# Performance work log

Hardware: AMD Instinct MI355X
Metric: run time of the kernel (lower is better)

Reference implementation:

```python
import jax, jax.numpy as jnp
import numpy as np
import math

NUM_HEADS = 16
HIDDEN = 1024
MLP = 4096
SEQ = 2048
HEAD_DIM = HIDDEN // NUM_HEADS  # 64
EPS = 1e-5


def setup_inputs() -> dict:
    key = jax.random.key(0)
    ks = jax.random.split(key, 16)
    s = 0.02
    inp = {
        "x": jax.random.normal(ks[0], (SEQ, HIDDEN), jnp.float32),
        "rope_cos": jnp.cos(jnp.arange(SEQ, dtype=jnp.float32)[:, None] * (1.0 / (10000.0 ** (jnp.arange(HEAD_DIM // 2, dtype=jnp.float32) * 2 / HEAD_DIM)))[None, :]),
        "rope_sin": jnp.sin(jnp.arange(SEQ, dtype=jnp.float32)[:, None] * (1.0 / (10000.0 ** (jnp.arange(HEAD_DIM // 2, dtype=jnp.float32) * 2 / HEAD_DIM)))[None, :]),
        "norm0_w": jnp.ones((HIDDEN,), jnp.float32),
        "norm0_b": jnp.zeros((HIDDEN,), jnp.float32),
        "norm1_w": jnp.ones((HIDDEN,), jnp.float32),
        "norm1_b": jnp.zeros((HIDDEN,), jnp.float32),
        "wqkv_w": jax.random.normal(ks[1], (3 * HIDDEN, HIDDEN), jnp.float32) * s,
        "wqkv_b": jnp.zeros((3 * HIDDEN,), jnp.float32),
        "wo_w": jax.random.normal(ks[2], (HIDDEN, HIDDEN), jnp.float32) * s,
        "wo_b": jnp.zeros((HIDDEN,), jnp.float32),
        "up_w": jax.random.normal(ks[3], (MLP, HIDDEN), jnp.float32) * s,
        "up_b": jnp.zeros((MLP,), jnp.float32),
        "down_w": jax.random.normal(ks[4], (HIDDEN, MLP), jnp.float32) * s,
        "down_b": jnp.zeros((HIDDEN,), jnp.float32),
        # 4 packed sequences of length 512 each
        "input_row_offsets": jnp.array([0, 512, 1024, 1536, 2048], jnp.int32),
    }
    return inp


def _layernorm(x, w, b):
    m = jnp.mean(x, axis=-1, keepdims=True)
    v = jnp.mean((x - m) ** 2, axis=-1, keepdims=True)
    return (x - m) * jax.lax.rsqrt(v + EPS) * w + b


def _rope(t, cos, sin):
    # t: [S, nh, hd]; cos/sin: [S, hd/2] -> complex rotation of adjacent pairs
    S, nh, hd = t.shape
    t2 = t.reshape(S, nh, hd // 2, 2)
    re, im = t2[..., 0], t2[..., 1]
    c = cos[:, None, :]
    s = sin[:, None, :]
    out = jnp.stack([re * c - im * s, re * s + im * c], axis=-1)
    return out.reshape(S, nh, hd)


def _block(x, rope_cos, rope_sin, norm0_w, norm0_b, wqkv_w, wqkv_b, wo_w, wo_b,
           up_w, up_b, down_w, down_b, norm1_w, norm1_b, input_row_offsets):
    S, H = x.shape
    nh, hd = NUM_HEADS, HEAD_DIM
    h = _layernorm(x, norm0_w, norm0_b)
    qkv = (h @ wqkv_w.T + wqkv_b).reshape(S, 3, nh, hd)
    q, k, v = qkv[:, 0], qkv[:, 1], qkv[:, 2]
    q = _rope(q, rope_cos, rope_sin)
    k = _rope(k, rope_cos, rope_sin)
    # block-diagonal bool mask added as 0/1 float (matches torch `attn_weight += bool_mask`)
    seg = jnp.searchsorted(input_row_offsets, jnp.arange(S), side="right") - 1
    mask = (seg[:, None] == seg[None, :]).astype(jnp.float32)  # [S, S]
    scores = jnp.einsum("shd,thd->hst", q, k) / math.sqrt(hd) + mask[None]
    attn = jax.nn.softmax(scores.astype(jnp.float32), axis=-1).astype(q.dtype)
    out = jnp.einsum("hst,thd->shd", attn, v).reshape(S, H)
    x = x + (out @ wo_w.T + wo_b)
    h = _layernorm(x, norm1_w, norm1_b)
    h = jax.nn.gelu(h @ up_w.T + up_b, approximate=True)
    return x + (h @ down_w.T + down_b)


def reference(x, rope_cos, rope_sin, norm0_w, norm0_b, norm1_w, norm1_b,
              wqkv_w, wqkv_b, wo_w, wo_b, up_w, up_b, down_w, down_b,
              input_row_offsets):
    return _block(x, rope_cos, rope_sin, norm0_w, norm0_b, wqkv_w, wqkv_b,
                  wo_w, wo_b, up_w, up_b, down_w, down_b, norm1_w, norm1_b,
                  input_row_offsets)
```

## Files before the change

kernel.cpp:

```cpp
#include <hip/hip_runtime.h>
#include <hip/hip_bf16.h>
#include <math.h>

#define SEQ 2048
#define HID 1024
#define NH 16
#define HD 64

using f32x4  = __attribute__((ext_vector_type(4))) float;
using bf16x8 = __attribute__((ext_vector_type(8))) short;

union U8 { unsigned int u[4]; bf16x8 v; short s[8]; };

__device__ __forceinline__ short f2bf(float f) {
  unsigned int x = __float_as_uint(f);
  unsigned int r = (x + 0x7fffu + ((x >> 16) & 1u)) >> 16;
  return (short)(r & 0xffffu);
}

__device__ __forceinline__ unsigned int pkbf(float a, float b) {
  return ((unsigned int)(unsigned short)f2bf(a)) |
         (((unsigned int)(unsigned short)f2bf(b)) << 16);
}

__device__ __forceinline__ float bf2f_lo(unsigned int u) {
  return __uint_as_float((u & 0xffffu) << 16);
}
__device__ __forceinline__ float bf2f_hi(unsigned int u) {
  return __uint_as_float(u & 0xffff0000u);
}

__device__ __forceinline__ float fast_exp2(float x) {
#if __has_builtin(__builtin_amdgcn_exp2f)
  return __builtin_amdgcn_exp2f(x);
#else
  return exp2f(x);
#endif
}

__device__ __forceinline__ float fast_rcp(float x) {
#if __has_builtin(__builtin_amdgcn_rcpf)
  return __builtin_amdgcn_rcpf(x);
#else
  return 1.0f / x;
#endif
}

__device__ __forceinline__ void async_cp16(const void* g, void* l) {
  __builtin_amdgcn_global_load_lds(
      (__attribute__((address_space(1))) void*)(g),
      (__attribute__((address_space(3))) void*)(l), 16, 0, 0);
}

__global__ void cvt_all_kernel(const float* __restrict__ a, const float* __restrict__ b,
                               const float* __restrict__ c, const float* __restrict__ d,
                               short* __restrict__ oa, short* __restrict__ ob,
                               short* __restrict__ oc, short* __restrict__ od) {
  int i = blockIdx.x * blockDim.x + threadIdx.x;
  const float* src; short* dst; int off;
  if (i < 786432)        { src = a; dst = oa; off = i; }
  else if (i < 1048576)  { src = b; dst = ob; off = i - 786432; }
  else if (i < 2097152)  { src = c; dst = oc; off = i - 1048576; }
  else                   { src = d; dst = od; off = i - 2097152; }
  float4 v = ((const float4*)src)[off];
  short4 o;
  o.x = f2bf(v.x); o.y = f2bf(v.y); o.z = f2bf(v.z); o.w = f2bf(v.w);
  ((short4*)dst)[off] = o;
}

__global__ __launch_bounds__(256) void ln_kernel(const float* __restrict__ x,
    const float* __restrict__ w, const float* __restrict__ b, short* __restrict__ out) {
  int row = blockIdx.x;
  int tid = threadIdx.x;
  float4 v = ((const float4*)(x + (size_t)row * HID))[tid];
  float s  = v.x + v.y + v.z + v.w;
  float s2 = v.x*v.x + v.y*v.y + v.z*v.z + v.w*v.w;
#pragma unroll
  for (int o = 32; o >= 1; o >>= 1) {
    s  += __shfl_xor(s,  o);
    s2 += __shfl_xor(s2, o);
  }
  __shared__ float red[8];
  int wv = tid >> 6;
  if ((tid & 63) == 0) { red[wv] = s; red[4 + wv] = s2; }
  __syncthreads();
  float ts  = red[0] + red[1] + red[2] + red[3];
  float ts2 = red[4] + red[5] + red[6] + red[7];
  float mean = ts * (1.0f / HID);
  float var  = ts2 * (1.0f / HID) - mean * mean;
  float rs = rsqrtf(var + 1e-5f);
  float4 wv4 = ((const float4*)w)[tid];
  float4 bv4 = ((const float4*)b)[tid];
  short4 o;
  o.x = f2bf((v.x - mean) * rs * wv4.x + bv4.x);
  o.y = f2bf((v.y - mean) * rs * wv4.y + bv4.y);
  o.z = f2bf((v.z - mean) * rs * wv4.z + bv4.z);
  o.w = f2bf((v.w - mean) * rs * wv4.w + bv4.w);
  ((short4*)(out + (size_t)row * HID))[tid] = o;
}

__global__ void rope_qk_kernel(const short* __restrict__ qkvb,
    const float* __restrict__ cosb, const float* __restrict__ sinb,
    short* __restrict__ Qh, short* __restrict__ Kh) {
  int tid = blockIdx.x * blockDim.x + threadIdx.x;
  int s   = tid >> 10;
  int r   = tid & 1023;
  int j   = r >> 9;
  int rem = r & 511;
  int h   = rem >> 5;
  int i   = rem & 31;
  int d   = i * 2;
  unsigned int u = *(const unsigned int*)(qkvb + (size_t)s * 3072 + j * 1024 + h * 64 + d);
  float a = bf2f_lo(u), b = bf2f_hi(u);
  float c  = cosb[s * 32 + i];
  float sn = sinb[s * 32 + i];
  float scale = (j == 0) ? 0.18033688011112043f : 1.0f;
  unsigned int o = pkbf(scale * (a * c - b * sn), scale * (a * sn + b * c));
  short* dst = (j == 0 ? Qh : Kh) + ((size_t)h * SEQ + s) * HD + d;
  *(unsigned int*)dst = o;
}

__global__ __launch_bounds__(256) void vtrans_kernel(const short* __restrict__ qkvb,
                                                     short* __restrict__ Vt) {
  __shared__ short tile[64 * 72];
  int s0   = blockIdx.x * 64;
  int head = blockIdx.y;
  int tid  = threadIdx.x;
#pragma unroll
  for (int p = 0; p < 2; p++) {
    int seg = p * 256 + tid;
    int row = seg >> 3;
    int c8  = seg & 7;
    bf16x8 v = *(const bf16x8*)(qkvb + (size_t)(s0 + row) * 3072 + 2048 + head * 64 + c8 * 8);
    *(bf16x8*)(tile + row * 72 + c8 * 8) = v;
  }
  __syncthreads();
#pragma unroll
  for (int p = 0; p < 2; p++) {
    int seg = p * 256 + tid;
    int d   = seg >> 3;
    int sc  = seg & 7;
    U8 o;
#pragma unroll
    for (int j = 0; j < 8; j++) o.s[j] = tile[(sc * 8 + j) * 72 + d];
    *(bf16x8*)(Vt + ((size_t)head * HD + d) * SEQ + s0 + sc * 8) = o.v;
  }
}

template <int EPI>
__global__ __launch_bounds__(256) void gemm_bt_kernel(
    const short* __restrict__ A, const short* __restrict__ B,
    const float* __restrict__ bias, const float* __restrict__ resid,
    void* __restrict__ outp, int M, int N, int Klen, int Kstride) {
  __shared__ __attribute__((aligned(16))) short Alds[128 * 32];
  __shared__ __attribute__((aligned(16))) short Blds[128 * 32];
  int tid = threadIdx.x;
  int w    = tid >> 6;
  int lane = tid & 63;
  int lcol  = lane & 15;
  int lhalf = lane >> 4;
  int m0 = blockIdx.y * 128;
  int n0 = blockIdx.x * 128;
  int z  = blockIdx.z;
  int wm = (w & 1) * 64;
  int wn = (w >> 1) * 64;

  const short* apt[2];
  const short* bpt[2];
#pragma unroll
  for (int p = 0; p < 2; p++) {
    int seg = p * 256 + tid;
    int row = seg >> 2;
    int c   = (seg & 3) ^ ((row >> 1) & 3);
    apt[p] = A + (size_t)z * Klen + (size_t)(m0 + row) * Kstride + c * 8;
    bpt[p] = B + (size_t)z * Klen + (size_t)(n0 + row) * Kstride + c * 8;
  }
  int sw = (lhalf ^ ((lcol >> 1) & 3)) * 8;

  f32x4 acc[4][4];
#pragma unroll
  for (int i = 0; i < 4; i++)
#pragma unroll
    for (int j = 0; j < 4; j++) acc[i][j] = (f32x4){0.f, 0.f, 0.f, 0.f};

  for (int k0 = 0; k0 < Klen; k0 += 32) {
#pragma unroll
    for (int p = 0; p < 2; p++) {
      async_cp16(apt[p], Alds + p * 2048 + w * 512);  apt[p] += 32;
      async_cp16(bpt[p], Blds + p * 2048 + w * 512);  bpt[p] += 32;
    }
    __syncthreads();
    bf16x8 af[4], bfr[4];
#pragma unroll
    for (int i = 0; i < 4; i++)
      af[i] = *(const bf16x8*)(Alds + (wm + i * 16 + lcol) * 32 + sw);
#pragma unroll
    for (int j = 0; j < 4; j++)
      bfr[j] = *(const bf16x8*)(Blds + (wn + j * 16 + lcol) * 32 + sw);
#pragma unroll
    for (int i = 0; i < 4; i++)
#pragma unroll
      for (int j = 0; j < 4; j++)
        acc[i][j] = __builtin_amdgcn_mfma_f32_16x16x32_bf16(af[i], bfr[j], acc[i][j], 0, 0, 0);
    __syncthreads();
  }

  float* outf = (float*)outp + (EPI == 4 ? (size_t)z * M * N : 0);
#pragma unroll
  for (int i = 0; i < 4; i++) {
#pragma unroll
    for (int j = 0; j < 4; j++) {
#pragma unroll
      for (int r = 0; r < 4; r++) {
        int row = m0 + wm + i * 16 + lhalf * 4 + r;
        int col = n0 + wn + j * 16 + lcol;
        float v = acc[i][j][r];
        if (EPI != 4) v += bias[col];
        if (EPI == 2) {
          float t = v * (1.5957691216057308f + 0.07135481283942279f * v * v);
          float e = fast_exp2(t * -1.4426950408889634f);
          v = v * fast_rcp(1.0f + e);
          ((short*)outp)[(size_t)row * N + col] = f2bf(v);
        } else if (EPI == 3) {
          ((short*)outp)[(size_t)row * N + col] = f2bf(v);
        } else {
          outf[(size_t)row * N + col] = v;
        }
      }
    }
  }
}

__global__ __launch_bounds__(256) void attn_kernel(
    const short* __restrict__ Qh, const short* __restrict__ Kh,
    const short* __restrict__ Vt, const int* __restrict__ offs,
    float* __restrict__ Opart, float* __restrict__ Lpart) {
  __shared__ __attribute__((aligned(16))) short Klds[64 * 64];
  __shared__ __attribute__((aligned(16))) short Vlds[64 * 64];
  __shared__ __attribute__((aligned(16))) unsigned int Plds[4][16 * 34];
  int head = blockIdx.y;
  int q0   = blockIdx.x * 64;
  int z    = blockIdx.z;
  int tid  = threadIdx.x;
  int w    = tid >> 6;
  int lane = tid & 63;
  int lcol = lane & 15;
  int h    = lane >> 4;
  int o1 = offs[1], o2 = offs[2], o3 = offs[3];

  int qrow = q0 + w * 16 + lcol;
  const short* qb = Qh + ((size_t)head * SEQ + qrow) * HD;
  bf16x8 qf0 = *(const bf16x8*)(qb + h * 8);
  bf16x8 qf1 = *(const bf16x8*)(qb + 32 + h * 8);
  int sq = (qrow >= o1) + (qrow >= o2) + (qrow >= o3);
  U8 qe;
  qe.u[0] = 0; qe.u[1] = 0; qe.u[2] = 0; qe.u[3] = 0;
  if (h == 0) qe.s[sq] = (short)0x3FB9;
  bf16x8 qf2 = qe.v;

  bf16x8 ones;
#pragma unroll
  for (int i = 0; i < 8; i++) ones[i] = 0x3F80;

  int tbeg = z * 1024;
  const short* kp0; const short* kp1; const short* vp0; const short* vp1;
  {
    int seg = tid, row = seg >> 3, g = (seg & 7) ^ (row & 7);
    kp0 = Kh + ((size_t)head * SEQ + tbeg + row) * HD + g * 8;
    vp0 = Vt + ((size_t)head * HD + row) * SEQ + tbeg + g * 8;
    seg = 256 + tid; row = seg >> 3; g = (seg & 7) ^ (row & 7);
    kp1 = Kh + ((size_t)head * SEQ + tbeg + row) * HD + g * 8;
    vp1 = Vt + ((size_t)head * HD + row) * SEQ + tbeg + g * 8;
  }

  f32x4 o_acc[4];
#pragma unroll
  for (int nt = 0; nt < 4; nt++) o_acc[nt] = (f32x4){0.f, 0.f, 0.f, 0.f};
  f32x4 acc_l = (f32x4){0.f, 0.f, 0.f, 0.f};

  for (int t0 = 0; t0 < 1024; t0 += 64) {
    async_cp16(kp0, Klds + w * 512);          kp0 += 64 * HD;
    async_cp16(kp1, Klds + 2048 + w * 512);   kp1 += 64 * HD;
    async_cp16(vp0, Vlds + w * 512);          vp0 += 64;
    async_cp16(vp1, Vlds + 2048 + w * 512);   vp1 += 64;
    __syncthreads();

#pragma unroll
    for (int n = 0; n < 4; n++) {
      int krow = n * 16 + lcol;
      int r7 = krow & 7;
      const short* ka = Klds + krow * 64;
      bf16x8 kf0 = *(const bf16x8*)(ka + (h ^ r7) * 8);
      bf16x8 kf1 = *(const bf16x8*)(ka + ((4 + h) ^ r7) * 8);
      int key = tbeg + t0 + krow;
      int sk = (key >= o1) + (key >= o2) + (key >= o3);
      U8 ke;
      ke.u[0] = (h == 0) ? ((sk == 0) ? 0x00003F80u : (sk == 1) ? 0x3F800000u : 0u) : 0u;
      ke.u[1] = (h == 0) ? ((sk == 2) ? 0x00003F80u : (sk == 3) ? 0x3F800000u : 0u) : 0u;
      ke.u[2] = 0; ke.u[3] = 0;
      f32x4 sacc = (f32x4){0.f, 0.f, 0.f, 0.f};
      sacc = __builtin_amdgcn_mfma_f32_16x16x32_bf16(kf0, qf0, sacc, 0, 0, 0);
      sacc = __builtin_amdgcn_mfma_f32_16x16x32_bf16(kf1, qf1, sacc, 0, 0, 0);
      sacc = __builtin_amdgcn_mfma_f32_16x16x32_bf16(ke.v, qf2, sacc, 0, 0, 0);
      float p0 = fast_exp2(sacc[0]);
      float p1 = fast_exp2(sacc[1]);
      float p2 = fast_exp2(sacc[2]);
      float p3 = fast_exp2(sacc[3]);
      uint2 pw;
      pw.x = __builtin_amdgcn_perm(__float_as_uint(p1), __float_as_uint(p0), 0x07060302);
      pw.y = __builtin_amdgcn_perm(__float_as_uint(p3), __float_as_uint(p2), 0x07060302);
      *(uint2*)&Plds[w][lcol * 34 + n * 8 + h * 2] = pw;
    }

#pragma unroll
    for (int kc = 0; kc < 2; kc++) {
      int base = lcol * 34 + kc * 16 + h * 4;
      uint2 a = *(const uint2*)&Plds[w][base];
      uint2 b = *(const uint2*)&Plds[w][base + 2];
      U8 pu;
      pu.u[0] = a.x; pu.u[1] = a.y; pu.u[2] = b.x; pu.u[3] = b.y;
#pragma unroll
      for (int nt = 0; nt < 4; nt++) {
        int vrow = nt * 16 + lcol;
        bf16x8 vf = *(const bf16x8*)(Vlds + vrow * 64 + (((kc * 4 + h) ^ (vrow & 7)) * 8));
        o_acc[nt] = __builtin_amdgcn_mfma_f32_16x16x32_bf16(vf, pu.v, o_acc[nt], 0, 0, 0);
      }
      acc_l = __builtin_amdgcn_mfma_f32_16x16x32_bf16(ones, pu.v, acc_l, 0, 0, 0);
    }
    __syncthreads();
  }

  float* op = Opart + (size_t)z * SEQ * HID + (size_t)qrow * HID + head * HD + h * 4;
#pragma unroll
  for (int nt = 0; nt < 4; nt++)
    *(f32x4*)(op + nt * 16) = o_acc[nt];
  if (lane < 16)
    Lpart[((size_t)z * NH + head) * SEQ + qrow] = acc_l[0];
}

__global__ __launch_bounds__(256) void attn_merge_kernel(
    const float* __restrict__ Opart, const float* __restrict__ Lpart,
    short* __restrict__ attn) {
  int i = blockIdx.x * blockDim.x + threadIdx.x;
  int col4 = i & 255;
  int row  = i >> 8;
  int head = col4 >> 4;
  float4 a = ((const float4*)Opart)[i];
  float4 b = ((const float4*)(Opart + (size_t)SEQ * HID))[i];
  float l = Lpart[(size_t)head * SEQ + row] + Lpart[(size_t)(NH + head) * SEQ + row];
  float rl = 1.0f / l;
  short4 o;
  o.x = f2bf((a.x + b.x) * rl);
  o.y = f2bf((a.y + b.y) * rl);
  o.z = f2bf((a.z + b.z) * rl);
  o.w = f2bf((a.w + b.w) * rl);
  ((short4*)attn)[i] = o;
}

__global__ __launch_bounds__(256) void merge_ln_kernel(
    const float* __restrict__ part, const float* __restrict__ bias,
    const float* __restrict__ resid, const float* __restrict__ w,
    const float* __restrict__ b, float* __restrict__ x1, short* __restrict__ h1) {
  int row = blockIdx.x;
  int tid = threadIdx.x;
  size_t idx = (size_t)row * HID / 4 + tid;
  float4 v = ((const float4*)part)[idx];
#pragma unroll
  for (int z = 1; z < 4; z++) {
    float4 q = ((const float4*)part)[(size_t)z * SEQ * HID / 4 + idx];
    v.x += q.x; v.y += q.y; v.z += q.z; v.w += q.w;
  }
  float4 bi = ((const float4*)bias)[tid];
  float4 rs4 = ((const float4*)(resid + (size_t)row * HID))[tid];
  v.x += bi.x + rs4.x; v.y += bi.y + rs4.y; v.z += bi.z + rs4.z; v.w += bi.w + rs4.w;
  ((float4*)(x1 + (size_t)row * HID))[tid] = v;
  float s  = v.x + v.y + v.z + v.w;
  float s2 = v.x*v.x + v.y*v.y + v.z*v.z + v.w*v.w;
#pragma unroll
  for (int o = 32; o >= 1; o >>= 1) {
    s  += __shfl_xor(s,  o);
    s2 += __shfl_xor(s2, o);
  }
  __shared__ float red[8];
  int wv = tid >> 6;
  if ((tid & 63) == 0) { red[wv] = s; red[4 + wv] = s2; }
  __syncthreads();
  float ts  = red[0] + red[1] + red[2] + red[3];
  float ts2 = red[4] + red[5] + red[6] + red[7];
  float mean = ts * (1.0f / HID);
  float var  = ts2 * (1.0f / HID) - mean * mean;
  float rsq = rsqrtf(var + 1e-5f);
  float4 wv4 = ((const float4*)w)[tid];
  float4 bv4 = ((const float4*)b)[tid];
  short4 o;
  o.x = f2bf((v.x - mean) * rsq * wv4.x + bv4.x);
  o.y = f2bf((v.y - mean) * rsq * wv4.y + bv4.y);
  o.z = f2bf((v.z - mean) * rsq * wv4.z + bv4.z);
  o.w = f2bf((v.w - mean) * rsq * wv4.w + bv4.w);
  ((short4*)(h1 + (size_t)row * HID))[tid] = o;
}

__global__ __launch_bounds__(256) void merge_bias_kernel(
    const float* __restrict__ part, const float* __restrict__ bias,
    const float* __restrict__ resid, float* __restrict__ out) {
  int i = blockIdx.x * blockDim.x + threadIdx.x;
  int col4 = i & 255;
  float4 v = ((const float4*)part)[i];
#pragma unroll
  for (int z = 1; z < 4; z++) {
    float4 q = ((const float4*)part)[(size_t)z * SEQ * HID / 4 + i];
    v.x += q.x; v.y += q.y; v.z += q.z; v.w += q.w;
  }
  float4 bi = ((const float4*)bias)[col4];
  float4 rs = ((const float4*)resid)[i];
  float4 o;
  o.x = v.x + bi.x + rs.x;
  o.y = v.y + bi.y + rs.y;
  o.z = v.z + bi.z + rs.z;
  o.w = v.w + bi.w + rs.w;
  ((float4*)out)[i] = o;
}

extern "C" void kernel_launch(void* const* d_in, const int* in_sizes, int n_in,
                              void* d_out, int out_size, void* d_ws, size_t ws_size,
                              hipStream_t stream) {
  const float* x      = (const float*)d_in[0];
  const float* ropec  = (const float*)d_in[1];
  const float* ropes  = (const float*)d_in[2];
  const float* n0w    = (const float*)d_in[3];
  const float* n0b    = (const float*)d_in[4];
  const float* n1w    = (const float*)d_in[5];
  const float* n1b    = (const float*)d_in[6];
  const float* wqkv_w = (const float*)d_in[7];
  const float* wqkv_b = (const float*)d_in[8];
  const float* wo_w   = (const float*)d_in[9];
  const float* wo_b   = (const float*)d_in[10];
  const float* up_w   = (const float*)d_in[11];
  const float* up_b   = (const float*)d_in[12];
  const float* down_w = (const float*)d_in[13];
  const float* down_b = (const float*)d_in[14];
  const int*   offs   = (const int*)d_in[15];
  float* out = (float*)d_out;

  char* base = (char*)d_ws;
  short* wqkv_bf = (short*)(base + 0);
  short* wo_bf   = (short*)(base + 6291456);
  short* up_bf   = (short*)(base + 8388608);
  short* down_bf = (short*)(base + 16777216);
  short* h0      = (short*)(base + 25165824);
  short* qkv_bf  = (short*)(base + 29360128);
  short* Qh      = (short*)(base + 41943040);
  short* Kh      = (short*)(base + 46137344);
  short* Vt      = (short*)(base + 50331648);
  float* Apart   = (float*)(base + 54525952);
  float* Lpart   = (float*)(base + 71303168);
  short* attn    = (short*)(base + 71565312);
  float* x1      = (float*)(base + 75759616);
  short* h1      = (short*)(base + 84148224);
  float* wopart  = (float*)(base + 25165824);
  short* u       = (short*)(base + 25165824);
  float* dnpart  = (float*)(base + 41943040);

  cvt_all_kernel<<<12288, 256, 0, stream>>>(wqkv_w, wo_w, up_w, down_w,
                                            wqkv_bf, wo_bf, up_bf, down_bf);
  ln_kernel<<<2048, 256, 0, stream>>>(x, n0w, n0b, h0);
  gemm_bt_kernel<3><<<dim3(24, 16), 256, 0, stream>>>(h0, wqkv_bf, wqkv_b, nullptr,
                                                      qkv_bf, 2048, 3072, 1024, 1024);
  rope_qk_kernel<<<8192, 256, 0, stream>>>(qkv_bf, ropec, ropes, Qh, Kh);
  vtrans_kernel<<<dim3(32, 16), 256, 0, stream>>>(qkv_bf, Vt);
  attn_kernel<<<dim3(32, 16, 2), 256, 0, stream>>>(Qh, Kh, Vt, offs, Apart, Lpart);
  attn_merge_kernel<<<2048, 256, 0, stream>>>(Apart, Lpart, attn);
  gemm_bt_kernel<4><<<dim3(8, 16, 4), 256, 0, stream>>>(attn, wo_bf, nullptr, nullptr,
                                                        wopart, 2048, 1024, 256, 1024);
  merge_ln_kernel<<<2048, 256, 0, stream>>>(wopart, wo_b, x, n1w, n1b, x1, h1);
  gemm_bt_kernel<2><<<dim3(32, 16), 256, 0, stream>>>(h1, up_bf, up_b, nullptr,
                                                      u, 2048, 4096, 1024, 1024);
  gemm_bt_kernel<4><<<dim3(8, 16, 4), 256, 0, stream>>>(u, down_bf, nullptr, nullptr,
                                                        dnpart, 2048, 1024, 1024, 4096);
  merge_bias_kernel<<<2048, 256, 0, stream>>>(dnpart, down_b, x1, out);
}
```

Baseline: 299.7 us.

## Restructure attention: 128-row Q tiles, register-resident P via 16x16x16 MFMA, bf16 partials

The attention kernel now handles 128 query rows per block, as two 64-row sets, so each K/V tile loaded into LDS is reused twice. The LDS round-trip for P is removed by feeding the exp'd scores straight into 16x16x16 bf16 MFMAs whose operand layout matches the score accumulator. The key range is split into 4 chunks instead of 2, and partial outputs are stored as bf16 rather than fp32, roughly halving merge traffic. The costs are more registers per thread, more MFMA instructions of smaller shape, and a small loss of precision in the partial sums.

```diff
diff --git a/kernel.cpp b/kernel.cpp
--- a/kernel.cpp
+++ b/kernel.cpp
@@ -9,8 +9,21 @@
 
 using f32x4  = __attribute__((ext_vector_type(4))) float;
 using bf16x8 = __attribute__((ext_vector_type(8))) short;
+using bf16x4 = __attribute__((ext_vector_type(4))) short;
 
 union U8 { unsigned int u[4]; bf16x8 v; short s[8]; };
+union U4 { unsigned int u[2]; bf16x4 v; short s[4]; };
+
+#if __has_builtin(__builtin_amdgcn_mfma_f32_16x16x16bf16_1k)
+#define MFMA16(a, b, c) __builtin_amdgcn_mfma_f32_16x16x16bf16_1k(a, b, c, 0, 0, 0)
+#else
+__device__ __forceinline__ f32x4 mfma16_asm(bf16x4 a, bf16x4 b, f32x4 c) {
+  asm volatile("v_mfma_f32_16x16x16_bf16 %0, %1, %2, %0\n\ts_nop 7\n\ts_nop 7"
+               : "+v"(c) : "v"(a), "v"(b));
+  return c;
+}
+#define MFMA16(a, b, c) mfma16_asm(a, b, c)
+#endif
 
 __device__ __forceinline__ short f2bf(float f) {
   unsigned int x = __float_as_uint(f);
@@ -234,35 +247,47 @@
 __global__ __launch_bounds__(256) void attn_kernel(
     const short* __restrict__ Qh, const short* __restrict__ Kh,
     const short* __restrict__ Vt, const int* __restrict__ offs,
-    float* __restrict__ Opart, float* __restrict__ Lpart) {
+    short* __restrict__ Opart, float* __restrict__ Lpart) {
   __shared__ __attribute__((aligned(16))) short Klds[64 * 64];
   __shared__ __attribute__((aligned(16))) short Vlds[64 * 64];
-  __shared__ __attribute__((aligned(16))) unsigned int Plds[4][16 * 34];
   int head = blockIdx.y;
-  int q0   = blockIdx.x * 64;
+  int q0   = blockIdx.x * 128;
   int z    = blockIdx.z;
   int tid  = threadIdx.x;
   int w    = tid >> 6;
   int lane = tid & 63;
   int lcol = lane & 15;
   int h    = lane >> 4;
+  int s7   = lcol & 7;
   int o1 = offs[1], o2 = offs[2], o3 = offs[3];
 
-  int qrow = q0 + w * 16 + lcol;
-  const short* qb = Qh + ((size_t)head * SEQ + qrow) * HD;
-  bf16x8 qf0 = *(const bf16x8*)(qb + h * 8);
-  bf16x8 qf1 = *(const bf16x8*)(qb + 32 + h * 8);
-  int sq = (qrow >= o1) + (qrow >= o2) + (qrow >= o3);
-  U8 qe;
-  qe.u[0] = 0; qe.u[1] = 0; qe.u[2] = 0; qe.u[3] = 0;
-  if (h == 0) qe.s[sq] = (short)0x3FB9;
-  bf16x8 qf2 = qe.v;
-
-  bf16x8 ones;
-#pragma unroll
-  for (int i = 0; i < 8; i++) ones[i] = 0x3F80;
-
-  int tbeg = z * 1024;
+  int qrowA = q0 + w * 16 + lcol;
+  int qrowB = qrowA + 64;
+  const short* qbA = Qh + ((size_t)head * SEQ + qrowA) * HD;
+  const short* qbB = Qh + ((size_t)head * SEQ + qrowB) * HD;
+  bf16x8 qf0a = *(const bf16x8*)(qbA + h * 8);
+  bf16x8 qf1a = *(const bf16x8*)(qbA + 32 + h * 8);
+  bf16x8 qf0b = *(const bf16x8*)(qbB + h * 8);
+  bf16x8 qf1b = *(const bf16x8*)(qbB + 32 + h * 8);
+  int sqA = (qrowA >= o1) + (qrowA >= o2) + (qrowA >= o3);
+  int sqB = (qrowB >= o1) + (qrowB >= o2) + (qrowB >= o3);
+  U8 qeA, qeB;
+#pragma unroll
+  for (int i = 0; i < 4; i++) { qeA.u[i] = 0; qeB.u[i] = 0; }
+  if (h == 0) { qeA.s[sqA] = (short)0x3FB9; qeB.s[sqB] = (short)0x3FB9; }
+
+  bf16x4 ones4;
+#pragma unroll
+  for (int i = 0; i < 4; i++) ones4[i] = (short)0x3F80;
+
+  int kbase0 = lcol * 64 + ((h ^ s7) * 8);
+  int kbase1 = lcol * 64 + (((4 + h) ^ s7) * 8);
+  int vbase[4];
+#pragma unroll
+  for (int n = 0; n < 4; n++)
+    vbase[n] = lcol * 64 + (((n * 2 + (h >> 1)) ^ s7) * 8) + (h & 1) * 4;
+
+  int tbeg = z * 512;
   const short* kp0; const short* kp1; const short* vp0; const short* vp1;
   {
     int seg = tid, row = seg >> 3, g = (seg & 7) ^ (row & 7);
@@ -273,12 +298,16 @@
     vp1 = Vt + ((size_t)head * HD + row) * SEQ + tbeg + g * 8;
   }
 
-  f32x4 o_acc[4];
-#pragma unroll
-  for (int nt = 0; nt < 4; nt++) o_acc[nt] = (f32x4){0.f, 0.f, 0.f, 0.f};
-  f32x4 acc_l = (f32x4){0.f, 0.f, 0.f, 0.f};
-
-  for (int t0 = 0; t0 < 1024; t0 += 64) {
+  f32x4 oA[4], oB[4];
+#pragma unroll
+  for (int nt = 0; nt < 4; nt++) {
+    oA[nt] = (f32x4){0.f, 0.f, 0.f, 0.f};
+    oB[nt] = (f32x4){0.f, 0.f, 0.f, 0.f};
+  }
+  f32x4 lA = (f32x4){0.f, 0.f, 0.f, 0.f};
+  f32x4 lB = (f32x4){0.f, 0.f, 0.f, 0.f};
+
+  for (int t0 = 0; t0 < 512; t0 += 64) {
     async_cp16(kp0, Klds + w * 512);          kp0 += 64 * HD;
     async_cp16(kp1, Klds + 2048 + w * 512);   kp1 += 64 * HD;
     async_cp16(vp0, Vlds + w * 512);          vp0 += 64;
@@ -287,74 +316,82 @@
 
 #pragma unroll
     for (int n = 0; n < 4; n++) {
-      int krow = n * 16 + lcol;
-      int r7 = krow & 7;
-      const short* ka = Klds + krow * 64;
-      bf16x8 kf0 = *(const bf16x8*)(ka + (h ^ r7) * 8);
-      bf16x8 kf1 = *(const bf16x8*)(ka + ((4 + h) ^ r7) * 8);
-      int key = tbeg + t0 + krow;
+      bf16x8 kf0 = *(const bf16x8*)(Klds + n * 1024 + kbase0);
+      bf16x8 kf1 = *(const bf16x8*)(Klds + n * 1024 + kbase1);
+      int key = tbeg + t0 + n * 16 + lcol;
       int sk = (key >= o1) + (key >= o2) + (key >= o3);
       U8 ke;
       ke.u[0] = (h == 0) ? ((sk == 0) ? 0x00003F80u : (sk == 1) ? 0x3F800000u : 0u) : 0u;
       ke.u[1] = (h == 0) ? ((sk == 2) ? 0x00003F80u : (sk == 3) ? 0x3F800000u : 0u) : 0u;
       ke.u[2] = 0; ke.u[3] = 0;
-      f32x4 sacc = (f32x4){0.f, 0.f, 0.f, 0.f};
-      sacc = __builtin_amdgcn_mfma_f32_16x16x32_bf16(kf0, qf0, sacc, 0, 0, 0);
-      sacc = __builtin_amdgcn_mfma_f32_16x16x32_bf16(kf1, qf1, sacc, 0, 0, 0);
-      sacc = __builtin_amdgcn_mfma_f32_16x16x32_bf16(ke.v, qf2, sacc, 0, 0, 0);
-      float p0 = fast_exp2(sacc[0]);
-      float p1 = fast_exp2(sacc[1]);
-      float p2 = fast_exp2(sacc[2]);
-      float p3 = fast_exp2(sacc[3]);
-      uint2 pw;
-      pw.x = __builtin_amdgcn_perm(__float_as_uint(p1), __float_as_uint(p0), 0x07060302);
-      pw.y = __builtin_amdgcn_perm(__float_as_uint(p3), __float_as_uint(p2), 0x07060302);
-      *(uint2*)&Plds[w][lcol * 34 + n * 8 + h * 2] = pw;
-    }
-
-#pragma unroll
-    for (int kc = 0; kc < 2; kc++) {
-      int base = lcol * 34 + kc * 16 + h * 4;
-      uint2 a = *(const uint2*)&Plds[w][base];
-      uint2 b = *(const uint2*)&Plds[w][base + 2];
-      U8 pu;
-      pu.u[0] = a.x; pu.u[1] = a.y; pu.u[2] = b.x; pu.u[3] = b.y;
+
+      f32x4 sA = (f32x4){0.f, 0.f, 0.f, 0.f};
+      sA = __builtin_amdgcn_mfma_f32_16x16x32_bf16(kf0, qf0a, sA, 0, 0, 0);
+      sA = __builtin_amdgcn_mfma_f32_16x16x32_bf16(kf1, qf1a, sA, 0, 0, 0);
+      sA = __builtin_amdgcn_mfma_f32_16x16x32_bf16(ke.v, qeA.v, sA, 0, 0, 0);
+      f32x4 sB = (f32x4){0.f, 0.f, 0.f, 0.f};
+      sB = __builtin_amdgcn_mfma_f32_16x16x32_bf16(kf0, qf0b, sB, 0, 0, 0);
+      sB = __builtin_amdgcn_mfma_f32_16x16x32_bf16(kf1, qf1b, sB, 0, 0, 0);
+      sB = __builtin_amdgcn_mfma_f32_16x16x32_bf16(ke.v, qeB.v, sB, 0, 0, 0);
+
+      float a0 = fast_exp2(sA[0]), a1 = fast_exp2(sA[1]);
+      float a2 = fast_exp2(sA[2]), a3 = fast_exp2(sA[3]);
+      float b0 = fast_exp2(sB[0]), b1 = fast_exp2(sB[1]);
+      float b2 = fast_exp2(sB[2]), b3 = fast_exp2(sB[3]);
+      U4 pA, pB;
+      pA.u[0] = __builtin_amdgcn_perm(__float_as_uint(a1), __float_as_uint(a0), 0x07060302);
+      pA.u[1] = __builtin_amdgcn_perm(__float_as_uint(a3), __float_as_uint(a2), 0x07060302);
+      pB.u[0] = __builtin_amdgcn_perm(__float_as_uint(b1), __float_as_uint(b0), 0x07060302);
+      pB.u[1] = __builtin_amdgcn_perm(__float_as_uint(b3), __float_as_uint(b2), 0x07060302);
+
 #pragma unroll
       for (int nt = 0; nt < 4; nt++) {
-        int vrow = nt * 16 + lcol;
-        bf16x8 vf = *(const bf16x8*)(Vlds + vrow * 64 + (((kc * 4 + h) ^ (vrow & 7)) * 8));
-        o_acc[nt] = __builtin_amdgcn_mfma_f32_16x16x32_bf16(vf, pu.v, o_acc[nt], 0, 0, 0);
+        bf16x4 vf = *(const bf16x4*)(Vlds + nt * 1024 + vbase[n]);
+        oA[nt] = MFMA16(vf, pA.v, oA[nt]);
+        oB[nt] = MFMA16(vf, pB.v, oB[nt]);
       }
-      acc_l = __builtin_amdgcn_mfma_f32_16x16x32_bf16(ones, pu.v, acc_l, 0, 0, 0);
+      lA = MFMA16(ones4, pA.v, lA);
+      lB = MFMA16(ones4, pB.v, lB);
     }
     __syncthreads();
   }
 
-  float* op = Opart + (size_t)z * SEQ * HID + (size_t)qrow * HID + head * HD + h * 4;
-#pragma unroll
-  for (int nt = 0; nt < 4; nt++)
-    *(f32x4*)(op + nt * 16) = o_acc[nt];
-  if (lane < 16)
-    Lpart[((size_t)z * NH + head) * SEQ + qrow] = acc_l[0];
+  short* opA = Opart + ((size_t)z * SEQ + qrowA) * HID + head * HD + h * 4;
+  short* opB = Opart + ((size_t)z * SEQ + qrowB) * HID + head * HD + h * 4;
+#pragma unroll
+  for (int nt = 0; nt < 4; nt++) {
+    uint2 ua, ub;
+    ua.x = pkbf(oA[nt][0], oA[nt][1]); ua.y = pkbf(oA[nt][2], oA[nt][3]);
+    ub.x = pkbf(oB[nt][0], oB[nt][1]); ub.y = pkbf(oB[nt][2], oB[nt][3]);
+    *(uint2*)(opA + nt * 16) = ua;
+    *(uint2*)(opB + nt * 16) = ub;
+  }
+  if (lane < 16) {
+    Lpart[((size_t)z * NH + head) * SEQ + qrowA] = lA[0];
+    Lpart[((size_t)z * NH + head) * SEQ + qrowB] = lB[0];
+  }
 }
 
 __global__ __launch_bounds__(256) void attn_merge_kernel(
-    const float* __restrict__ Opart, const float* __restrict__ Lpart,
+    const short* __restrict__ Opart, const float* __restrict__ Lpart,
     short* __restrict__ attn) {
   int i = blockIdx.x * blockDim.x + threadIdx.x;
   int col4 = i & 255;
   int row  = i >> 8;
   int head = col4 >> 4;
-  float4 a = ((const float4*)Opart)[i];
-  float4 b = ((const float4*)(Opart + (size_t)SEQ * HID))[i];
-  float l = Lpart[(size_t)head * SEQ + row] + Lpart[(size_t)(NH + head) * SEQ + row];
-  float rl = 1.0f / l;
-  short4 o;
-  o.x = f2bf((a.x + b.x) * rl);
-  o.y = f2bf((a.y + b.y) * rl);
-  o.z = f2bf((a.z + b.z) * rl);
-  o.w = f2bf((a.w + b.w) * rl);
-  ((short4*)attn)[i] = o;
+  float acc0 = 0.f, acc1 = 0.f, acc2 = 0.f, acc3 = 0.f, l = 0.f;
+#pragma unroll
+  for (int zz = 0; zz < 4; zz++) {
+    uint2 p = ((const uint2*)(Opart + (size_t)zz * SEQ * HID))[i];
+    acc0 += bf2f_lo(p.x); acc1 += bf2f_hi(p.x);
+    acc2 += bf2f_lo(p.y); acc3 += bf2f_hi(p.y);
+    l += Lpart[((size_t)zz * NH + head) * SEQ + row];
+  }
+  float rl = fast_rcp(l);
+  uint2 o;
+  o.x = pkbf(acc0 * rl, acc1 * rl);
+  o.y = pkbf(acc2 * rl, acc3 * rl);
+  ((uint2*)attn)[i] = o;
 }
 
 __global__ __launch_bounds__(256) void merge_ln_kernel(
@@ -452,11 +489,11 @@
   short* Qh      = (short*)(base + 41943040);
   short* Kh      = (short*)(base + 46137344);
   short* Vt      = (short*)(base + 50331648);
-  float* Apart   = (float*)(base + 54525952);
+  short* Opart   = (short*)(base + 54525952);
   float* Lpart   = (float*)(base + 71303168);
-  short* attn    = (short*)(base + 71565312);
-  float* x1      = (float*)(base + 75759616);
-  short* h1      = (short*)(base + 84148224);
+  short* attn    = (short*)(base + 71827456);
+  float* x1      = (float*)(base + 76021760);
+  short* h1      = (short*)(base + 84410368);
   float* wopart  = (float*)(base + 25165824);
   short* u       = (short*)(base + 25165824);
   float* dnpart  = (float*)(base + 41943040);
@@ -468,8 +505,8 @@
                                                       qkv_bf, 2048, 3072, 1024, 1024);
   rope_qk_kernel<<<8192, 256, 0, stream>>>(qkv_bf, ropec, ropes, Qh, Kh);
   vtrans_kernel<<<dim3(32, 16), 256, 0, stream>>>(qkv_bf, Vt);
-  attn_kernel<<<dim3(32, 16, 2), 256, 0, stream>>>(Qh, Kh, Vt, offs, Apart, Lpart);
-  attn_merge_kernel<<<2048, 256, 0, stream>>>(Apart, Lpart, attn);
+  attn_kernel<<<dim3(16, 16, 4), 256, 0, stream>>>(Qh, Kh, Vt, offs, Opart, Lpart);
+  attn_merge_kernel<<<2048, 256, 0, stream>>>(Opart, Lpart, attn);
   gemm_bt_kernel<4><<<dim3(8, 16, 4), 256, 0, stream>>>(attn, wo_bf, nullptr, nullptr,
                                                         wopart, 2048, 1024, 256, 1024);
   merge_ln_kernel<<<2048, 256, 0, stream>>>(wopart, wo_b, x, n1w, n1b, x1, h1);
```

Result: slower. 313.2 us (+4.5%).

## Store split-K and split-KV partials in bf16, split attention keys four ways

Applied to the files above, without the earlier changes.

Split-K GEMM partials and attention partial outputs are now written as bf16 instead of fp32, and the merge kernels read them as bf16. The goal is to halve partial-buffer traffic. The attention kernel now splits keys across four z-slices instead of two, which doubles parallelism and shortens each block's loop. It also precomputes the swizzled LDS offsets once, outside the loop. In exchange, bf16 partial sums lose precision, and the attention merge reads four slices instead of two.

```diff
diff --git a/kernel.cpp b/kernel.cpp
--- a/kernel.cpp
+++ b/kernel.cpp
@@ -205,7 +205,6 @@
     __syncthreads();
   }
 
-  float* outf = (float*)outp + (EPI == 4 ? (size_t)z * M * N : 0);
 #pragma unroll
   for (int i = 0; i < 4; i++) {
 #pragma unroll
@@ -215,7 +214,7 @@
         int row = m0 + wm + i * 16 + lhalf * 4 + r;
         int col = n0 + wn + j * 16 + lcol;
         float v = acc[i][j][r];
-        if (EPI != 4) v += bias[col];
+        if (EPI != 5) v += bias[col];
         if (EPI == 2) {
           float t = v * (1.5957691216057308f + 0.07135481283942279f * v * v);
           float e = fast_exp2(t * -1.4426950408889634f);
@@ -224,7 +223,7 @@
         } else if (EPI == 3) {
           ((short*)outp)[(size_t)row * N + col] = f2bf(v);
         } else {
-          outf[(size_t)row * N + col] = v;
+          ((short*)outp)[(size_t)z * M * N + (size_t)row * N + col] = f2bf(v);
         }
       }
     }
@@ -234,7 +233,7 @@
 __global__ __launch_bounds__(256) void attn_kernel(
     const short* __restrict__ Qh, const short* __restrict__ Kh,
     const short* __restrict__ Vt, const int* __restrict__ offs,
-    float* __restrict__ Opart, float* __restrict__ Lpart) {
+    short* __restrict__ Opart, float* __restrict__ Lpart) {
   __shared__ __attribute__((aligned(16))) short Klds[64 * 64];
   __shared__ __attribute__((aligned(16))) short Vlds[64 * 64];
   __shared__ __attribute__((aligned(16))) unsigned int Plds[4][16 * 34];
@@ -246,6 +245,7 @@
   int lane = tid & 63;
   int lcol = lane & 15;
   int h    = lane >> 4;
+  int s7   = lcol & 7;
   int o1 = offs[1], o2 = offs[2], o3 = offs[3];
 
   int qrow = q0 + w * 16 + lcol;
@@ -256,13 +256,19 @@
   U8 qe;
   qe.u[0] = 0; qe.u[1] = 0; qe.u[2] = 0; qe.u[3] = 0;
   if (h == 0) qe.s[sq] = (short)0x3FB9;
-  bf16x8 qf2 = qe.v;
 
   bf16x8 ones;
 #pragma unroll
   for (int i = 0; i < 8; i++) ones[i] = 0x3F80;
 
-  int tbeg = z * 1024;
+  int kb0 = lcol * 64 + ((h ^ s7) * 8);
+  int kb1 = lcol * 64 + (((4 + h) ^ s7) * 8);
+  int vb0 = lcol * 64 + ((h ^ s7) * 8);
+  int vb1 = lcol * 64 + (((4 + h) ^ s7) * 8);
+  int pwb = lcol * 34 + h * 2;
+  int prb = lcol * 34 + h * 4;
+
+  int tbeg = z * 512;
   const short* kp0; const short* kp1; const short* vp0; const short* vp1;
   {
     int seg = tid, row = seg >> 3, g = (seg & 7) ^ (row & 7);
@@ -278,7 +284,7 @@
   for (int nt = 0; nt < 4; nt++) o_acc[nt] = (f32x4){0.f, 0.f, 0.f, 0.f};
   f32x4 acc_l = (f32x4){0.f, 0.f, 0.f, 0.f};
 
-  for (int t0 = 0; t0 < 1024; t0 += 64) {
+  for (int t0 = 0; t0 < 512; t0 += 64) {
     async_cp16(kp0, Klds + w * 512);          kp0 += 64 * HD;
     async_cp16(kp1, Klds + 2048 + w * 512);   kp1 += 64 * HD;
     async_cp16(vp0, Vlds + w * 512);          vp0 += 64;
@@ -287,21 +293,20 @@
 
 #pragma unroll
     for (int n = 0; n < 4; n++) {
-      int krow = n * 16 + lcol;
-      int r7 = krow & 7;
-      const short* ka = Klds + krow * 64;
-      bf16x8 kf0 = *(const bf16x8*)(ka + (h ^ r7) * 8);
-      bf16x8 kf1 = *(const bf16x8*)(ka + ((4 + h) ^ r7) * 8);
-      int key = tbeg + t0 + krow;
+      bf16x8 kf0 = *(const bf16x8*)(Klds + n * 1024 + kb0);
+      bf16x8 kf1 = *(const bf16x8*)(Klds + n * 1024 + kb1);
+      int key = tbeg + t0 + n * 16 + lcol;
       int sk = (key >= o1) + (key >= o2) + (key >= o3);
       U8 ke;
       ke.u[0] = (h == 0) ? ((sk == 0) ? 0x00003F80u : (sk == 1) ? 0x3F800000u : 0u) : 0u;
       ke.u[1] = (h == 0) ? ((sk == 2) ? 0x00003F80u : (sk == 3) ? 0x3F800000u : 0u) : 0u;
       ke.u[2] = 0; ke.u[3] = 0;
+
       f32x4 sacc = (f32x4){0.f, 0.f, 0.f, 0.f};
       sacc = __builtin_amdgcn_mfma_f32_16x16x32_bf16(kf0, qf0, sacc, 0, 0, 0);
       sacc = __builtin_amdgcn_mfma_f32_16x16x32_bf16(kf1, qf1, sacc, 0, 0, 0);
-      sacc = __builtin_amdgcn_mfma_f32_16x16x32_bf16(ke.v, qf2, sacc, 0, 0, 0);
+      sacc = __builtin_amdgcn_mfma_f32_16x16x32_bf16(ke.v, qe.v, sacc, 0, 0, 0);
+
       float p0 = fast_exp2(sacc[0]);
       float p1 = fast_exp2(sacc[1]);
       float p2 = fast_exp2(sacc[2]);
@@ -309,20 +314,19 @@
       uint2 pw;
       pw.x = __builtin_amdgcn_perm(__float_as_uint(p1), __float_as_uint(p0), 0x07060302);
       pw.y = __builtin_amdgcn_perm(__float_as_uint(p3), __float_as_uint(p2), 0x07060302);
-      *(uint2*)&Plds[w][lcol * 34 + n * 8 + h * 2] = pw;
+      *(uint2*)&Plds[w][pwb + n * 8] = pw;
     }
 
 #pragma unroll
     for (int kc = 0; kc < 2; kc++) {
-      int base = lcol * 34 + kc * 16 + h * 4;
-      uint2 a = *(const uint2*)&Plds[w][base];
-      uint2 b = *(const uint2*)&Plds[w][base + 2];
+      uint2 a = *(const uint2*)&Plds[w][prb + kc * 16];
+      uint2 b = *(const uint2*)&Plds[w][prb + kc * 16 + 2];
       U8 pu;
       pu.u[0] = a.x; pu.u[1] = a.y; pu.u[2] = b.x; pu.u[3] = b.y;
+      int vb = kc ? vb1 : vb0;
 #pragma unroll
       for (int nt = 0; nt < 4; nt++) {
-        int vrow = nt * 16 + lcol;
-        bf16x8 vf = *(const bf16x8*)(Vlds + vrow * 64 + (((kc * 4 + h) ^ (vrow & 7)) * 8));
+        bf16x8 vf = *(const bf16x8*)(Vlds + nt * 1024 + vb);
         o_acc[nt] = __builtin_amdgcn_mfma_f32_16x16x32_bf16(vf, pu.v, o_acc[nt], 0, 0, 0);
       }
       acc_l = __builtin_amdgcn_mfma_f32_16x16x32_bf16(ones, pu.v, acc_l, 0, 0, 0);
@@ -330,45 +334,53 @@
     __syncthreads();
   }
 
-  float* op = Opart + (size_t)z * SEQ * HID + (size_t)qrow * HID + head * HD + h * 4;
-#pragma unroll
-  for (int nt = 0; nt < 4; nt++)
-    *(f32x4*)(op + nt * 16) = o_acc[nt];
+  short* op = Opart + ((size_t)z * SEQ + qrow) * HID + head * HD + h * 4;
+#pragma unroll
+  for (int nt = 0; nt < 4; nt++) {
+    uint2 ua;
+    ua.x = pkbf(o_acc[nt][0], o_acc[nt][1]);
+    ua.y = pkbf(o_acc[nt][2], o_acc[nt][3]);
+    *(uint2*)(op + nt * 16) = ua;
+  }
   if (lane < 16)
     Lpart[((size_t)z * NH + head) * SEQ + qrow] = acc_l[0];
 }
 
 __global__ __launch_bounds__(256) void attn_merge_kernel(
-    const float* __restrict__ Opart, const float* __restrict__ Lpart,
+    const short* __restrict__ Opart, const float* __restrict__ Lpart,
     short* __restrict__ attn) {
   int i = blockIdx.x * blockDim.x + threadIdx.x;
   int col4 = i & 255;
   int row  = i >> 8;
   int head = col4 >> 4;
-  float4 a = ((const float4*)Opart)[i];
-  float4 b = ((const float4*)(Opart + (size_t)SEQ * HID))[i];
-  float l = Lpart[(size_t)head * SEQ + row] + Lpart[(size_t)(NH + head) * SEQ + row];
-  float rl = 1.0f / l;
-  short4 o;
-  o.x = f2bf((a.x + b.x) * rl);
-  o.y = f2bf((a.y + b.y) * rl);
-  o.z = f2bf((a.z + b.z) * rl);
-  o.w = f2bf((a.w + b.w) * rl);
-  ((short4*)attn)[i] = o;
+  float acc0 = 0.f, acc1 = 0.f, acc2 = 0.f, acc3 = 0.f, l = 0.f;
+#pragma unroll
+  for (int zz = 0; zz < 4; zz++) {
+    uint2 p = ((const uint2*)(Opart + (size_t)zz * SEQ * HID))[i];
+    acc0 += bf2f_lo(p.x); acc1 += bf2f_hi(p.x);
+    acc2 += bf2f_lo(p.y); acc3 += bf2f_hi(p.y);
+    l += Lpart[((size_t)zz * NH + head) * SEQ + row];
+  }
+  float rl = fast_rcp(l);
+  uint2 o;
+  o.x = pkbf(acc0 * rl, acc1 * rl);
+  o.y = pkbf(acc2 * rl, acc3 * rl);
+  ((uint2*)attn)[i] = o;
 }
 
 __global__ __launch_bounds__(256) void merge_ln_kernel(
-    const float* __restrict__ part, const float* __restrict__ bias,
+    const short* __restrict__ part, const float* __restrict__ bias,
     const float* __restrict__ resid, const float* __restrict__ w,
     const float* __restrict__ b, float* __restrict__ x1, short* __restrict__ h1) {
   int row = blockIdx.x;
   int tid = threadIdx.x;
   size_t idx = (size_t)row * HID / 4 + tid;
-  float4 v = ((const float4*)part)[idx];
-#pragma unroll
-  for (int z = 1; z < 4; z++) {
-    float4 q = ((const float4*)part)[(size_t)z * SEQ * HID / 4 + idx];
-    v.x += q.x; v.y += q.y; v.z += q.z; v.w += q.w;
+  float4 v = {0.f, 0.f, 0.f, 0.f};
+#pragma unroll
+  for (int z = 0; z < 4; z++) {
+    uint2 p = ((const uint2*)(part + (size_t)z * SEQ * HID))[idx];
+    v.x += bf2f_lo(p.x); v.y += bf2f_hi(p.x);
+    v.z += bf2f_lo(p.y); v.w += bf2f_hi(p.y);
   }
   float4 bi = ((const float4*)bias)[tid];
   float4 rs4 = ((const float4*)(resid + (size_t)row * HID))[tid];
@@ -401,15 +413,16 @@
 }
 
 __global__ __launch_bounds__(256) void merge_bias_kernel(
-    const float* __restrict__ part, const float* __restrict__ bias,
+    const short* __restrict__ part, const float* __restrict__ bias,
     const float* __restrict__ resid, float* __restrict__ out) {
   int i = blockIdx.x * blockDim.x + threadIdx.x;
   int col4 = i & 255;
-  float4 v = ((const float4*)part)[i];
-#pragma unroll
-  for (int z = 1; z < 4; z++) {
-    float4 q = ((const float4*)part)[(size_t)z * SEQ * HID / 4 + i];
-    v.x += q.x; v.y += q.y; v.z += q.z; v.w += q.w;
+  float4 v = {0.f, 0.f, 0.f, 0.f};
+#pragma unroll
+  for (int z = 0; z < 4; z++) {
+    uint2 p = ((const uint2*)(part + (size_t)z * SEQ * HID))[i];
+    v.x += bf2f_lo(p.x); v.y += bf2f_hi(p.x);
+    v.z += bf2f_lo(p.y); v.w += bf2f_hi(p.y);
   }
   float4 bi = ((const float4*)bias)[col4];
   float4 rs = ((const float4*)resid)[i];
@@ -452,14 +465,14 @@
   short* Qh      = (short*)(base + 41943040);
   short* Kh      = (short*)(base + 46137344);
   short* Vt      = (short*)(base + 50331648);
-  float* Apart   = (float*)(base + 54525952);
+  short* Opart   = (short*)(base + 54525952);
   float* Lpart   = (float*)(base + 71303168);
-  short* attn    = (short*)(base + 71565312);
-  float* x1      = (float*)(base + 75759616);
-  short* h1      = (short*)(base + 84148224);
-  float* wopart  = (float*)(base + 25165824);
+  short* attn    = (short*)(base + 71827456);
+  float* x1      = (float*)(base + 76021760);
+  short* h1      = (short*)(base + 84410368);
+  short* wopart  = (short*)(base + 25165824);
   short* u       = (short*)(base + 25165824);
-  float* dnpart  = (float*)(base + 41943040);
+  short* dnpart  = (short*)(base + 41943040);
 
   cvt_all_kernel<<<12288, 256, 0, stream>>>(wqkv_w, wo_w, up_w, down_w,
                                             wqkv_bf, wo_bf, up_bf, down_bf);
@@ -468,14 +481,14 @@
                                                       qkv_bf, 2048, 3072, 1024, 1024);
   rope_qk_kernel<<<8192, 256, 0, stream>>>(qkv_bf, ropec, ropes, Qh, Kh);
   vtrans_kernel<<<dim3(32, 16), 256, 0, stream>>>(qkv_bf, Vt);
-  attn_kernel<<<dim3(32, 16, 2), 256, 0, stream>>>(Qh, Kh, Vt, offs, Apart, Lpart);
-  attn_merge_kernel<<<2048, 256, 0, stream>>>(Apart, Lpart, attn);
-  gemm_bt_kernel<4><<<dim3(8, 16, 4), 256, 0, stream>>>(attn, wo_bf, nullptr, nullptr,
+  attn_kernel<<<dim3(32, 16, 4), 256, 0, stream>>>(Qh, Kh, Vt, offs, Opart, Lpart);
+  attn_merge_kernel<<<2048, 256, 0, stream>>>(Opart, Lpart, attn);
+  gemm_bt_kernel<5><<<dim3(8, 16, 4), 256, 0, stream>>>(attn, wo_bf, nullptr, nullptr,
                                                         wopart, 2048, 1024, 256, 1024);
   merge_ln_kernel<<<2048, 256, 0, stream>>>(wopart, wo_b, x, n1w, n1b, x1, h1);
   gemm_bt_kernel<2><<<dim3(32, 16), 256, 0, stream>>>(h1, up_bf, up_b, nullptr,
                                                       u, 2048, 4096, 1024, 1024);
-  gemm_bt_kernel<4><<<dim3(8, 16, 4), 256, 0, stream>>>(u, down_bf, nullptr, nullptr,
+  gemm_bt_kernel<5><<<dim3(8, 16, 4), 256, 0, stream>>>(u, down_bf, nullptr, nullptr,
                                                         dnpart, 2048, 1024, 1024, 4096);
   merge_bias_kernel<<<2048, 256, 0, stream>>>(dnpart, down_b, x1, out);
 }
```

Result: faster. 290.2 us (-3.2%).
